# Kernel optimization log

Hardware: AMD Instinct MI355X
Metric: run time of the kernel (lower is better)

The kernel has to match this reference:

```python
import jax, jax.numpy as jnp
import numpy as np

D = 4       # number of TT dimensions
N = 128     # mode size per dimension (Ns)
R = 16      # TT rank (RMAX)
B = 262144  # batch of query points


def setup_inputs() -> dict:
    key = jax.random.key(0)
    ks = jax.random.split(key, 5)
    # points in [-1, 1] (remap_needed=True assumes this domain)
    x = jax.random.uniform(ks[0], (B, D), dtype=jnp.float32) * 2.0 - 1.0
    core0 = jax.random.normal(ks[1], (1, N, R), dtype=jnp.float32)
    core1 = jax.random.normal(ks[2], (R, N, R), dtype=jnp.float32)
    core2 = jax.random.normal(ks[3], (R, N, R), dtype=jnp.float32)
    core3 = jax.random.normal(ks[4], (R, N, 1), dtype=jnp.float32)
    return {"x": x, "core0": core0, "core1": core1, "core2": core2, "core3": core3}


def _forward(x, cores):
    # remap: (x + 1) / 2 * (Ns[0] - 1)  (module uses Ns[0] for all dims)
    n0 = cores[0].shape[1]
    xr = (x + 1.0) * 0.5 * (n0 - 1)
    # per-dim clamp to [0, Ns[i]-1]
    ns = jnp.array([c.shape[1] for c in cores], dtype=x.dtype)  # [D]
    xc = jnp.clip(xr, 0.0, ns - 1.0)  # broadcast over D
    idx_low = jnp.floor(xc).astype(jnp.int32)   # [B, D]
    idx_high = jnp.ceil(xc).astype(jnp.int32)   # [B, D]
    wh = xc - idx_low.astype(x.dtype)           # [B, D] interpolation weights
    # gather + linear interpolation per core -> list of [r_prev, B, r_next]
    newcores = []
    for i, c in enumerate(cores):
        lo = jnp.take(c, idx_low[:, i], axis=1)   # [r_prev, B, r_next]
        hi = jnp.take(c, idx_high[:, i], axis=1)  # [r_prev, B, r_next]
        w = wh[:, i][None, :, None]               # [1, B, 1]
        newcores.append((1.0 - w) * lo + w * hi)
    # chained batched contraction, right to left (matches ttcontract)
    res = newcores[-1]
    for i in range(len(newcores) - 2, 0, -1):
        res = jnp.einsum('abc,cbk->abk', newcores[i], res)
    return jnp.einsum('abc,cbk->b', newcores[0], res)  # [B]


def reference(x, core0, core1, core2, core3):
    return _forward(x, [core0, core1, core2, core3])
```

## Files before the change

kernel.cpp:

```cpp
#include <hip/hip_runtime.h>
#include <hip/hip_bf16.h>

typedef unsigned int uint32;
typedef unsigned short u16;

#define NPT 128
#define RNK 16
#define MIDROW 264
#define MIDROW_U32 132
#define EDGEROW 20
#define SMEM_BYTES (2*NPT*MIDROW*2 + 2*NPT*EDGEROW*4)

#if defined(__has_builtin)
#if __has_builtin(__builtin_amdgcn_fdot2_f32_bf16)
#define HAVE_BFDOT2 1
#endif
#endif

__device__ __forceinline__ float bl(uint32 u){ return __uint_as_float(u << 16); }
__device__ __forceinline__ float bh(uint32 u){ return __uint_as_float(u & 0xffff0000u); }

#ifdef HAVE_BFDOT2
typedef __bf16 v2bf __attribute__((ext_vector_type(2)));
__device__ __forceinline__ v2bf bc(uint32 u){ return __builtin_bit_cast(v2bf, u); }

__device__ __forceinline__ float dot16b(const uint32* vp, uint4 U0, uint4 U1) {
  float s0 = 0.f, s1 = 0.f;
  s0 = __builtin_amdgcn_fdot2_f32_bf16(bc(vp[0]), bc(U0.x), s0, false);
  s0 = __builtin_amdgcn_fdot2_f32_bf16(bc(vp[1]), bc(U0.y), s0, false);
  s0 = __builtin_amdgcn_fdot2_f32_bf16(bc(vp[2]), bc(U0.z), s0, false);
  s0 = __builtin_amdgcn_fdot2_f32_bf16(bc(vp[3]), bc(U0.w), s0, false);
  s1 = __builtin_amdgcn_fdot2_f32_bf16(bc(vp[4]), bc(U1.x), s1, false);
  s1 = __builtin_amdgcn_fdot2_f32_bf16(bc(vp[5]), bc(U1.y), s1, false);
  s1 = __builtin_amdgcn_fdot2_f32_bf16(bc(vp[6]), bc(U1.z), s1, false);
  s1 = __builtin_amdgcn_fdot2_f32_bf16(bc(vp[7]), bc(U1.w), s1, false);
  return s0 + s1;
}
#else
__device__ __forceinline__ float dot16(const float* v, uint4 U0, uint4 U1) {
  float s0 = fmaf(v[1],  bh(U0.x), v[0]*bl(U0.x));
  s0 = fmaf(v[2],  bl(U0.y), s0); s0 = fmaf(v[3],  bh(U0.y), s0);
  float s1 = fmaf(v[5],  bh(U0.z), v[4]*bl(U0.z));
  s1 = fmaf(v[6],  bl(U0.w), s1); s1 = fmaf(v[7],  bh(U0.w), s1);
  float s2 = fmaf(v[9],  bh(U1.x), v[8]*bl(U1.x));
  s2 = fmaf(v[10], bl(U1.y), s2); s2 = fmaf(v[11], bh(U1.y), s2);
  float s3 = fmaf(v[13], bh(U1.z), v[12]*bl(U1.z));
  s3 = fmaf(v[14], bl(U1.w), s3); s3 = fmaf(v[15], bh(U1.w), s3);
  return (s0 + s1) + (s2 + s3);
}
#endif

__device__ __forceinline__ void tt_mid(const uint32* __restrict__ base, float xc, float v[16]) {
  int n0 = (int)xc;
  float w = xc - (float)n0;
  int n1 = min(n0 + 1, NPT - 1);
  const uint32* r0 = base + n0 * MIDROW_U32;
  const uint32* r1 = base + n1 * MIDROW_U32;

#ifdef HAVE_BFDOT2
  uint32 vp[8];
#pragma unroll
  for (int k = 0; k < 8; ++k) {
    __hip_bfloat16 l = __float2bfloat16(v[2*k]);
    __hip_bfloat16 h = __float2bfloat16(v[2*k+1]);
    vp[k] = (uint32)(*(u16*)&l) | ((uint32)(*(u16*)&h) << 16);
  }
#endif

  float nv[16];
#pragma unroll
  for (int j = 0; j < 16; ++j) {
    const uint4* p0 = (const uint4*)(r0 + j * 8);
    const uint4* p1 = (const uint4*)(r1 + j * 8);
    uint4 A0 = p0[0], A1 = p0[1];
    uint4 B0 = p1[0], B1 = p1[1];
#ifdef HAVE_BFDOT2
    float a = dot16b(vp, A0, A1);
    float b = dot16b(vp, B0, B1);
#else
    float a = dot16(v, A0, A1);
    float b = dot16(v, B0, B1);
#endif
    nv[j] = fmaf(w, b - a, a);
  }
#pragma unroll
  for (int j = 0; j < 16; ++j) v[j] = nv[j];
}

__device__ __forceinline__ float remap_clamp(float x) {
  float xr = (x + 1.0f) * 0.5f * (float)(NPT - 1);
  return fminf(fmaxf(xr, 0.0f), (float)(NPT - 1));
}

__global__ __launch_bounds__(1024, 4) void tt_kernel(
    const float* __restrict__ x,  const float* __restrict__ g0,
    const float* __restrict__ g1, const float* __restrict__ g2,
    const float* __restrict__ g3, float* __restrict__ out, int npts)
{
  extern __shared__ char smem[];
  unsigned short* c1 = (unsigned short*)smem;
  unsigned short* c2 = c1 + NPT * MIDROW;
  float* c0 = (float*)(c2 + NPT * MIDROW);
  float* c3 = c0 + NPT * EDGEROW;

  for (int t = threadIdx.x; t < RNK * NPT * RNK; t += blockDim.x) {
    int i = t >> 11;
    int n = (t >> 4) & (NPT - 1);
    int j = t & (RNK - 1);
    __hip_bfloat16 h1 = __float2bfloat16(g1[t]);
    __hip_bfloat16 h2 = __float2bfloat16(g2[t]);
    c1[n * MIDROW + j * 16 + i] = *(u16*)&h1;
    c2[n * MIDROW + j * 16 + i] = *(u16*)&h2;
  }
  for (int t = threadIdx.x; t < NPT * RNK; t += blockDim.x) {
    int n = t >> 4;
    int i = t & (RNK - 1);
    c0[n * EDGEROW + i] = g0[t];
    c3[n * EDGEROW + i] = g3[i * NPT + n];
  }
  __syncthreads();

  int p = blockIdx.x * blockDim.x + threadIdx.x;
  if (p >= npts) return;
  float4 xv = reinterpret_cast<const float4*>(x)[p];

  float v[16];
  {
    float xc = remap_clamp(xv.x);
    int n0 = (int)xc; float w = xc - (float)n0; int n1 = min(n0 + 1, NPT - 1);
    const float4* L = (const float4*)(c0 + n0 * EDGEROW);
    const float4* H = (const float4*)(c0 + n1 * EDGEROW);
#pragma unroll
    for (int k = 0; k < 4; ++k) {
      float4 l = L[k], h = H[k];
      v[4*k+0] = fmaf(w, h.x - l.x, l.x);
      v[4*k+1] = fmaf(w, h.y - l.y, l.y);
      v[4*k+2] = fmaf(w, h.z - l.z, l.z);
      v[4*k+3] = fmaf(w, h.w - l.w, l.w);
    }
  }
  tt_mid((const uint32*)c1, remap_clamp(xv.y), v);
  tt_mid((const uint32*)c2, remap_clamp(xv.z), v);
  float acc;
  {
    float xc = remap_clamp(xv.w);
    int n0 = (int)xc; float w = xc - (float)n0; int n1 = min(n0 + 1, NPT - 1);
    const float4* L = (const float4*)(c3 + n0 * EDGEROW);
    const float4* H = (const float4*)(c3 + n1 * EDGEROW);
    float a0 = 0.f, a1 = 0.f, a2 = 0.f, a3 = 0.f;
#pragma unroll
    for (int k = 0; k < 4; ++k) {
      float4 l = L[k], h = H[k];
      a0 = fmaf(v[4*k+0], fmaf(w, h.x - l.x, l.x), a0);
      a1 = fmaf(v[4*k+1], fmaf(w, h.y - l.y, l.y), a1);
      a2 = fmaf(v[4*k+2], fmaf(w, h.z - l.z, l.z), a2);
      a3 = fmaf(v[4*k+3], fmaf(w, h.w - l.w, l.w), a3);
    }
    acc = (a0 + a1) + (a2 + a3);
  }
  out[p] = acc;
}

extern "C" void kernel_launch(void* const* d_in, const int* in_sizes, int n_in,
                              void* d_out, int out_size, void* d_ws, size_t ws_size,
                              hipStream_t stream) {
  const float* x  = (const float*)d_in[0];
  const float* g0 = (const float*)d_in[1];
  const float* g1 = (const float*)d_in[2];
  const float* g2 = (const float*)d_in[3];
  const float* g3 = (const float*)d_in[4];
  float* out = (float*)d_out;

  int B = in_sizes[0] / 4;
  hipFuncSetAttribute(reinterpret_cast<const void*>(tt_kernel),
                      hipFuncAttributeMaxDynamicSharedMemorySize, SMEM_BYTES);
  int block = 1024;
  int grid = (B + block - 1) / block;
  tt_kernel<<<grid, block, SMEM_BYTES, stream>>>(x, g0, g1, g2, g3, out, B);
}
```

Before: 83.27 us.

## Move core2 to a global bf16 workspace, prepared by a separate kernel

A small prep kernel converts core2 to a packed bf16 layout in the workspace once per launch. The main kernel then reads core2 from global/L2 memory, so only core1 is staged in LDS. This halves the per-block LDS fill and footprint, and the mid-core row padding shrinks from 264 to 260 with 8-byte LDS loads. The cost is 16-byte gathers from global memory per point for the second mid core, plus an extra kernel launch.

```diff
diff --git a/kernel.cpp b/kernel.cpp
--- a/kernel.cpp
+++ b/kernel.cpp
@@ -6,10 +6,12 @@
 
 #define NPT 128
 #define RNK 16
-#define MIDROW 264
-#define MIDROW_U32 132
+#define MIDROW_U16 260
+#define MIDROW_U32 130
 #define EDGEROW 20
-#define SMEM_BYTES (2*NPT*MIDROW*2 + 2*NPT*EDGEROW*4)
+#define SMEM_G (NPT*MIDROW_U16*2 + 2*NPT*EDGEROW*4)
+#define SMEM_L (2*NPT*MIDROW_U16*2 + 2*NPT*EDGEROW*4)
+#define WS_NEEDED (RNK*NPT*RNK*2)
 
 #if defined(__has_builtin)
 #if __has_builtin(__builtin_amdgcn_fdot2_f32_bf16)
@@ -24,63 +26,94 @@
 typedef __bf16 v2bf __attribute__((ext_vector_type(2)));
 __device__ __forceinline__ v2bf bc(uint32 u){ return __builtin_bit_cast(v2bf, u); }
 
-__device__ __forceinline__ float dot16b(const uint32* vp, uint4 U0, uint4 U1) {
+__device__ __forceinline__ float dot16b(const uint32* vp, const uint32* u) {
   float s0 = 0.f, s1 = 0.f;
-  s0 = __builtin_amdgcn_fdot2_f32_bf16(bc(vp[0]), bc(U0.x), s0, false);
-  s0 = __builtin_amdgcn_fdot2_f32_bf16(bc(vp[1]), bc(U0.y), s0, false);
-  s0 = __builtin_amdgcn_fdot2_f32_bf16(bc(vp[2]), bc(U0.z), s0, false);
-  s0 = __builtin_amdgcn_fdot2_f32_bf16(bc(vp[3]), bc(U0.w), s0, false);
-  s1 = __builtin_amdgcn_fdot2_f32_bf16(bc(vp[4]), bc(U1.x), s1, false);
-  s1 = __builtin_amdgcn_fdot2_f32_bf16(bc(vp[5]), bc(U1.y), s1, false);
-  s1 = __builtin_amdgcn_fdot2_f32_bf16(bc(vp[6]), bc(U1.z), s1, false);
-  s1 = __builtin_amdgcn_fdot2_f32_bf16(bc(vp[7]), bc(U1.w), s1, false);
+#pragma unroll
+  for (int k = 0; k < 4; ++k) {
+    s0 = __builtin_amdgcn_fdot2_f32_bf16(bc(vp[k]),   bc(u[k]),   s0, false);
+    s1 = __builtin_amdgcn_fdot2_f32_bf16(bc(vp[4+k]), bc(u[4+k]), s1, false);
+  }
   return s0 + s1;
 }
 #else
-__device__ __forceinline__ float dot16(const float* v, uint4 U0, uint4 U1) {
-  float s0 = fmaf(v[1],  bh(U0.x), v[0]*bl(U0.x));
-  s0 = fmaf(v[2],  bl(U0.y), s0); s0 = fmaf(v[3],  bh(U0.y), s0);
-  float s1 = fmaf(v[5],  bh(U0.z), v[4]*bl(U0.z));
-  s1 = fmaf(v[6],  bl(U0.w), s1); s1 = fmaf(v[7],  bh(U0.w), s1);
-  float s2 = fmaf(v[9],  bh(U1.x), v[8]*bl(U1.x));
-  s2 = fmaf(v[10], bl(U1.y), s2); s2 = fmaf(v[11], bh(U1.y), s2);
-  float s3 = fmaf(v[13], bh(U1.z), v[12]*bl(U1.z));
-  s3 = fmaf(v[14], bl(U1.w), s3); s3 = fmaf(v[15], bh(U1.w), s3);
-  return (s0 + s1) + (s2 + s3);
-}
-#endif
-
-__device__ __forceinline__ void tt_mid(const uint32* __restrict__ base, float xc, float v[16]) {
+__device__ __forceinline__ float dot16f(const float* v, const uint32* u) {
+  float s0 = 0.f, s1 = 0.f;
+#pragma unroll
+  for (int k = 0; k < 4; ++k) {
+    s0 = fmaf(v[2*k],   bl(u[k]),   s0); s0 = fmaf(v[2*k+1],   bh(u[k]),   s0);
+    s1 = fmaf(v[8+2*k], bl(u[4+k]), s1); s1 = fmaf(v[9+2*k],   bh(u[4+k]), s1);
+  }
+  return s0 + s1;
+}
+#endif
+
+struct VPack {
+#ifdef HAVE_BFDOT2
+  uint32 p[8];
+  __device__ __forceinline__ void pack(const float v[16]) {
+#pragma unroll
+    for (int k = 0; k < 8; ++k) {
+      __hip_bfloat16 l = __float2bfloat16(v[2*k]);
+      __hip_bfloat16 h = __float2bfloat16(v[2*k+1]);
+      p[k] = (uint32)(*(u16*)&l) | ((uint32)(*(u16*)&h) << 16);
+    }
+  }
+  __device__ __forceinline__ float dot(const float* v, const uint32* u) const {
+    (void)v; return dot16b(p, u);
+  }
+#else
+  __device__ __forceinline__ void pack(const float v[16]) {}
+  __device__ __forceinline__ float dot(const float* v, const uint32* u) const {
+    return dot16f(v, u);
+  }
+#endif
+};
+
+__device__ __forceinline__ void tt_mid_lds(const uint32* __restrict__ base, float xc, float v[16]) {
   int n0 = (int)xc;
   float w = xc - (float)n0;
   int n1 = min(n0 + 1, NPT - 1);
   const uint32* r0 = base + n0 * MIDROW_U32;
   const uint32* r1 = base + n1 * MIDROW_U32;
-
-#ifdef HAVE_BFDOT2
-  uint32 vp[8];
-#pragma unroll
-  for (int k = 0; k < 8; ++k) {
-    __hip_bfloat16 l = __float2bfloat16(v[2*k]);
-    __hip_bfloat16 h = __float2bfloat16(v[2*k+1]);
-    vp[k] = (uint32)(*(u16*)&l) | ((uint32)(*(u16*)&h) << 16);
-  }
-#endif
-
+  VPack vp; vp.pack(v);
   float nv[16];
 #pragma unroll
   for (int j = 0; j < 16; ++j) {
-    const uint4* p0 = (const uint4*)(r0 + j * 8);
-    const uint4* p1 = (const uint4*)(r1 + j * 8);
-    uint4 A0 = p0[0], A1 = p0[1];
-    uint4 B0 = p1[0], B1 = p1[1];
-#ifdef HAVE_BFDOT2
-    float a = dot16b(vp, A0, A1);
-    float b = dot16b(vp, B0, B1);
-#else
-    float a = dot16(v, A0, A1);
-    float b = dot16(v, B0, B1);
-#endif
+    uint32 A[8], B[8];
+    const uint2* q0 = (const uint2*)(r0 + j * 8);
+    const uint2* q1 = (const uint2*)(r1 + j * 8);
+#pragma unroll
+    for (int m = 0; m < 4; ++m) {
+      uint2 a = q0[m]; A[2*m] = a.x; A[2*m+1] = a.y;
+      uint2 b = q1[m]; B[2*m] = b.x; B[2*m+1] = b.y;
+    }
+    float a = vp.dot(v, A);
+    float b = vp.dot(v, B);
+    nv[j] = fmaf(w, b - a, a);
+  }
+#pragma unroll
+  for (int j = 0; j < 16; ++j) v[j] = nv[j];
+}
+
+__device__ __forceinline__ void tt_mid_glb(const uint32* __restrict__ base, float xc, float v[16]) {
+  int n0 = (int)xc;
+  float w = xc - (float)n0;
+  int n1 = min(n0 + 1, NPT - 1);
+  const uint32* r0 = base + n0 * 128;
+  const uint32* r1 = base + n1 * 128;
+  VPack vp; vp.pack(v);
+  float nv[16];
+#pragma unroll
+  for (int j = 0; j < 16; ++j) {
+    uint32 A[8], B[8];
+    const uint4* q0 = (const uint4*)(r0 + j * 8);
+    const uint4* q1 = (const uint4*)(r1 + j * 8);
+    uint4 a0 = q0[0], a1 = q0[1];
+    uint4 b0 = q1[0], b1 = q1[1];
+    A[0]=a0.x; A[1]=a0.y; A[2]=a0.z; A[3]=a0.w; A[4]=a1.x; A[5]=a1.y; A[6]=a1.z; A[7]=a1.w;
+    B[0]=b0.x; B[1]=b0.y; B[2]=b0.z; B[3]=b0.w; B[4]=b1.x; B[5]=b1.y; B[6]=b1.z; B[7]=b1.w;
+    float a = vp.dot(v, A);
+    float b = vp.dot(v, B);
     nv[j] = fmaf(w, b - a, a);
   }
 #pragma unroll
@@ -92,15 +125,26 @@
   return fminf(fmaxf(xr, 0.0f), (float)(NPT - 1));
 }
 
+__global__ void prep_c2(const float* __restrict__ g2, uint32* __restrict__ ws) {
+  int o2 = blockIdx.x * blockDim.x + threadIdx.x;
+  int o = o2 * 2;
+  int n = o >> 8, j = (o >> 4) & 15, i = o & 15;
+  __hip_bfloat16 l = __float2bfloat16(g2[i * 2048 + n * 16 + j]);
+  __hip_bfloat16 h = __float2bfloat16(g2[(i + 1) * 2048 + n * 16 + j]);
+  ws[o2] = (uint32)(*(u16*)&l) | ((uint32)(*(u16*)&h) << 16);
+}
+
+template <bool C2GLOBAL>
 __global__ __launch_bounds__(1024, 4) void tt_kernel(
     const float* __restrict__ x,  const float* __restrict__ g0,
     const float* __restrict__ g1, const float* __restrict__ g2,
-    const float* __restrict__ g3, float* __restrict__ out, int npts)
+    const float* __restrict__ g3, const uint32* __restrict__ wsc2,
+    float* __restrict__ out, int npts)
 {
   extern __shared__ char smem[];
-  unsigned short* c1 = (unsigned short*)smem;
-  unsigned short* c2 = c1 + NPT * MIDROW;
-  float* c0 = (float*)(c2 + NPT * MIDROW);
+  u16* c1 = (u16*)smem;
+  u16* c2 = C2GLOBAL ? nullptr : c1 + NPT * MIDROW_U16;
+  float* c0 = (float*)(smem + (C2GLOBAL ? NPT*MIDROW_U16*2 : 2*NPT*MIDROW_U16*2));
   float* c3 = c0 + NPT * EDGEROW;
 
   for (int t = threadIdx.x; t < RNK * NPT * RNK; t += blockDim.x) {
@@ -108,9 +152,11 @@
     int n = (t >> 4) & (NPT - 1);
     int j = t & (RNK - 1);
     __hip_bfloat16 h1 = __float2bfloat16(g1[t]);
-    __hip_bfloat16 h2 = __float2bfloat16(g2[t]);
-    c1[n * MIDROW + j * 16 + i] = *(u16*)&h1;
-    c2[n * MIDROW + j * 16 + i] = *(u16*)&h2;
+    c1[n * MIDROW_U16 + j * 16 + i] = *(u16*)&h1;
+    if (!C2GLOBAL) {
+      __hip_bfloat16 h2 = __float2bfloat16(g2[t]);
+      c2[n * MIDROW_U16 + j * 16 + i] = *(u16*)&h2;
+    }
   }
   for (int t = threadIdx.x; t < NPT * RNK; t += blockDim.x) {
     int n = t >> 4;
@@ -139,8 +185,9 @@
       v[4*k+3] = fmaf(w, h.w - l.w, l.w);
     }
   }
-  tt_mid((const uint32*)c1, remap_clamp(xv.y), v);
-  tt_mid((const uint32*)c2, remap_clamp(xv.z), v);
+  tt_mid_lds((const uint32*)c1, remap_clamp(xv.y), v);
+  if (C2GLOBAL) tt_mid_glb(wsc2, remap_clamp(xv.z), v);
+  else          tt_mid_lds((const uint32*)c2, remap_clamp(xv.z), v);
   float acc;
   {
     float xc = remap_clamp(xv.w);
@@ -172,9 +219,19 @@
   float* out = (float*)d_out;
 
   int B = in_sizes[0] / 4;
-  hipFuncSetAttribute(reinterpret_cast<const void*>(tt_kernel),
-                      hipFuncAttributeMaxDynamicSharedMemorySize, SMEM_BYTES);
   int block = 1024;
   int grid = (B + block - 1) / block;
-  tt_kernel<<<grid, block, SMEM_BYTES, stream>>>(x, g0, g1, g2, g3, out, B);
-}
+
+  if (ws_size >= WS_NEEDED) {
+    hipFuncSetAttribute(reinterpret_cast<const void*>(tt_kernel<true>),
+                        hipFuncAttributeMaxDynamicSharedMemorySize, SMEM_G);
+    prep_c2<<<64, 256, 0, stream>>>(g2, (uint32*)d_ws);
+    tt_kernel<true><<<grid, block, SMEM_G, stream>>>(
+        x, g0, g1, g2, g3, (const uint32*)d_ws, out, B);
+  } else {
+    hipFuncSetAttribute(reinterpret_cast<const void*>(tt_kernel<false>),
+                        hipFuncAttributeMaxDynamicSharedMemorySize, SMEM_L);
+    tt_kernel<false><<<grid, block, SMEM_L, stream>>>(
+        x, g0, g1, g2, g3, nullptr, out, B);
+  }
+}
```

Measured after the change: 108.5 us. 1.3x slower.
